# Kernel tuning notes

Hardware: AMD Instinct MI355X
Metric: run time of the kernel (lower is better)

The kernel has to match this reference:

```python
import jax, jax.numpy as jnp
import numpy as np
from jax import lax

B, C, H, W = 1, 128, 56, 56
NH, NG, KS = 4, 1, 3
CG = C // NG          # channels per group
CH = C // NH          # channels per head
NHG = NH // NG        # heads per group
SCALE = CH ** -0.5


def _norm_grid(h, w, n):
    # matches _get_normalized_grid: (y, x) order, each normalized to [-1, 1]
    y = jnp.arange(h, dtype=jnp.float32) / (h - 1.0) * 2.0 - 1.0
    x = jnp.arange(w, dtype=jnp.float32) / (w - 1.0) * 2.0 - 1.0
    g = jnp.stack(jnp.meshgrid(y, x, indexing='ij'), axis=-1)  # (h, w, 2)
    return jnp.broadcast_to(g[None], (n, h, w, 2))


def _grid_sample(img, grid):
    # F.grid_sample: bilinear, align_corners=True, zeros padding; grid is (x, y) in [-1, 1]
    n, c, hi, wi = img.shape
    gs = grid.shape[1:-1]
    gx = grid[..., 0].reshape(n, -1)
    gy = grid[..., 1].reshape(n, -1)
    fx = (gx + 1.0) * 0.5 * (wi - 1)
    fy = (gy + 1.0) * 0.5 * (hi - 1)
    x0 = jnp.floor(fx)
    y0 = jnp.floor(fy)
    wx = fx - x0
    wy = fy - y0
    x0 = x0.astype(jnp.int32)
    y0 = y0.astype(jnp.int32)
    imgf = img.reshape(n, c, hi * wi)

    def corner(xi, yi, wgt):
        valid = (xi >= 0) & (xi < wi) & (yi >= 0) & (yi < hi)
        idx = jnp.clip(yi, 0, hi - 1) * wi + jnp.clip(xi, 0, wi - 1)
        vals = jax.vmap(lambda im, ii: jnp.take(im, ii, axis=1))(imgf, idx)  # (n, c, P)
        return vals * (wgt * valid)[:, None, :]

    out = (corner(x0, y0, (1 - wx) * (1 - wy)) + corner(x0 + 1, y0, wx * (1 - wy))
           + corner(x0, y0 + 1, (1 - wx) * wy) + corner(x0 + 1, y0 + 1, wx * wy))
    return out.reshape((n, c) + gs)


def _conv1x1(t, w, b):
    return jnp.einsum('bchw,oc->bohw', t, w) + b[None, :, None, None]


def _forward(x, query, dw_w, dw_b, ln_w, ln_b, pw_w, k_w, k_b, v_w, v_b, out_w, out_b, rpe_table):
    # conv_offset: depthwise 3x3 (stride 1, pad 1) -> channel LayerNorm -> GELU -> 1x1 to 2ch (no bias)
    qg = query.reshape(B * NG, CG, H, W)
    t = lax.conv_general_dilated(qg, dw_w, (1, 1), ((1, 1), (1, 1)),
                                 dimension_numbers=('NCHW', 'OIHW', 'NCHW'),
                                 feature_group_count=CG) + dw_b[None, :, None, None]
    mu = t.mean(axis=1, keepdims=True)
    var = ((t - mu) ** 2).mean(axis=1, keepdims=True)
    t = (t - mu) / jnp.sqrt(var + 1e-5) * ln_w[None, :, None, None] + ln_b[None, :, None, None]
    t = jax.nn.gelu(t, approximate=False)
    offset = jnp.einsum('bchw,oc->bohw', t, pw_w)  # (BG, 2, Hk, Wk) in (y, x) order
    Hk, Wk = offset.shape[-2:]
    n_sample = Hk * Wk

    # tanh-scaled offsets (scale_offset_range=True, factor 0.5)
    rng = jnp.array([1.0 / (Hk - 1.0), 1.0 / (Wk - 1.0)], jnp.float32).reshape(1, 2, 1, 1)
    offset = jnp.tanh(offset) * rng * 0.5
    offset = jnp.transpose(offset, (0, 2, 3, 1))  # (BG, Hk, Wk, 2)

    ref = _norm_grid(Hk, Wk, B * NG)
    rwo = offset + ref  # no clamp in the scale_offset_range branch

    # sample K/V features at deformed locations
    xs = _grid_sample(x.reshape(B * NG, CG, H, W), rwo[..., ::-1])  # (BG, CG, Hk, Wk)
    xs = xs.reshape(B, C, 1, n_sample)

    q = query.reshape(B * NH, CH, H * W)
    k = _conv1x1(xs, k_w, k_b).reshape(B * NH, CH, n_sample)
    v = _conv1x1(xs, v_w, v_b).reshape(B * NH, CH, n_sample)

    attn = jnp.einsum('bcm,bcn->bmn', q, k) * SCALE  # (B*NH, HW, n_sample)

    # relative position bias via bilinear lookup of rpe_table at displacements
    rpe = jnp.broadcast_to(rpe_table[None], (B,) + rpe_table.shape).reshape(B * NG, NHG, 2 * H - 1, 2 * W - 1)
    qgrid = _norm_grid(H, W, B * NG)
    disp = (qgrid.reshape(B * NG, H * W, 2)[:, :, None, :]
            - rwo.reshape(B * NG, n_sample, 2)[:, None, :, :]) * 0.5  # (BG, HW, n_sample, 2)
    bias = _grid_sample(rpe, disp[..., ::-1]).reshape(B * NH, H * W, n_sample)

    attn = jax.nn.softmax(attn + bias, axis=2)
    out = jnp.einsum('bmn,bcn->bcm', attn, v).reshape(B, C, H, W)
    return _conv1x1(out, out_w, out_b)


def setup_inputs() -> dict:
    key = jax.random.key(0)
    ks = jax.random.split(key, 8)
    f = lambda k, sh, s=0.02: jax.random.normal(k, sh, jnp.float32) * s
    return {
        'x': jax.random.normal(ks[0], (B, C, H, W), jnp.float32),
        'query': jax.random.normal(ks[1], (B, C, H, W), jnp.float32),
        'dw_w': f(ks[2], (CG, 1, KS, KS)),
        'dw_b': jnp.zeros((CG,), jnp.float32),
        'ln_w': jnp.ones((CG,), jnp.float32),
        'ln_b': jnp.zeros((CG,), jnp.float32),
        'pw_w': f(ks[3], (2, CG)),
        'k_w': f(ks[4], (C, C)),
        'k_b': jnp.zeros((C,), jnp.float32),
        'v_w': f(ks[5], (C, C)),
        'v_b': jnp.zeros((C,), jnp.float32),
        'out_w': f(ks[6], (C, C)),
        'out_b': jnp.zeros((C,), jnp.float32),
        'rpe_table': f(ks[7], (NH, 2 * H - 1, 2 * W - 1), 0.01),
    }


def reference(x, query, dw_w, dw_b, ln_w, ln_b, pw_w, k_w, k_b, v_w, v_b, out_w, out_b, rpe_table):
    return _forward(x, query, dw_w, dw_b, ln_w, ln_b, pw_w, k_w, k_b, v_w, v_b, out_w, out_b, rpe_table)
```

## Files before the change

### kernel.cpp

```cpp
#include <hip/hip_runtime.h>
#include <hip/hip_bf16.h>
#include <math.h>

#define HH 56
#define WW 56
#define HW 3136
#define NHEAD 4
#define RP 111
#define TP 113
#define TPE 12769
#define SCALE 0.17677669529663687f
#define GHW 12544
#define NCHUNK 14
#define CLEN 224
#define NSTEP 7

typedef unsigned short ushortT;
typedef __attribute__((ext_vector_type(8))) short short8v;
typedef __attribute__((ext_vector_type(16))) float f32x16;

#define OFF_RWO  0u
#define OFF_AA   8192u
#define OFF_W4   12288u
#define OFF_KBF  24832u
#define OFF_VBF  225536u
#define OFF_QBF  426240u
#define OFF_ATT  626944u
#define OFF_KWT  1028352u
#define OFF_VWT  1044736u
#define OFF_OWT  1061120u
#define OFF_XT   1077504u
#define OFF_QT   1478912u
#define OFF_TP2  1880320u
#define OFF_PART 1982976u

__device__ __forceinline__ ushortT f2bf(float f) {
    unsigned u = __float_as_uint(f);
    u += 0x7fffu + ((u >> 16) & 1u);
    return (ushortT)(u >> 16);
}

__device__ __forceinline__ unsigned cvtpk(float lo, float hi) {
    unsigned r;
    asm("v_cvt_pk_bf16_f32 %0, %1, %2" : "=v"(r) : "v"(lo), "v"(hi));
    return r;
}

__global__ void prep_kernel(const float* __restrict__ a, const float* __restrict__ b,
                            const float* __restrict__ c, const float* __restrict__ rpe,
                            float* __restrict__ at, float* __restrict__ bt,
                            float* __restrict__ ct, float2* __restrict__ tp2) {
    int i = blockIdx.x * 256 + threadIdx.x;
    if (blockIdx.y < 3) {
        if (i >= 16384) return;
        const float* src = (blockIdx.y == 0) ? a : (blockIdx.y == 1) ? b : c;
        float* dst       = (blockIdx.y == 0) ? at : (blockIdx.y == 1) ? bt : ct;
        int o = i >> 7, cc = i & 127;
        dst[cc * 128 + o] = src[i];
    } else {
        if (i >= NHEAD * TPE) return;
        int hd = i / TPE, r = i % TPE;
        int py = r / TP, px = r % TP;
        float v0 = 0.f, v1 = 0.f;
        if (py >= 1 && py <= RP) {
            if (px >= 1 && px <= RP)     v0 = rpe[hd * RP * RP + (py - 1) * RP + (px - 1)];
            if (px + 1 >= 1 && px + 1 <= RP) v1 = rpe[hd * RP * RP + (py - 1) * RP + px];
        }
        tp2[i] = make_float2(v0, v1);
    }
}

__global__ __launch_bounds__(256) void tx_kernel(const float* __restrict__ x,
                                                 const float* __restrict__ query,
                                                 float* __restrict__ xT, float* __restrict__ qT,
                                                 ushortT* __restrict__ qbf) {
    const float* src = blockIdx.z ? query : x;
    float* dst       = blockIdx.z ? qT : xT;
    __shared__ float tile[32][33];
    int pt = blockIdx.x * 32;
    int ct = blockIdx.y * 32;
    int jj = threadIdx.x & 31, ii = threadIdx.x >> 5;
#pragma unroll
    for (int r = 0; r < 4; r++)
        tile[ii + r * 8][jj] = src[(ct + ii + r * 8) * HW + pt + jj];
    __syncthreads();
#pragma unroll
    for (int r = 0; r < 4; r++) {
        int p = pt + ii + r * 8, c = ct + jj;
        float val = tile[jj][ii + r * 8];
        dst[p * 128 + c] = val;
        if (blockIdx.z)
            qbf[(size_t)((c >> 5) * HW + p) * 32 + (c & 31)] = f2bf(val * SCALE);
    }
}

__device__ __forceinline__ float wave_sum(float v) {
#pragma unroll
    for (int o = 1; o < 64; o <<= 1) v += __shfl_xor(v, o);
    return v;
}

__global__ __launch_bounds__(128) void offset_kernel(
    const float* __restrict__ qT, const float* __restrict__ dww, const float* __restrict__ dwb,
    const float* __restrict__ lnw, const float* __restrict__ lnb, const float* __restrict__ pww,
    float* __restrict__ rwo, int* __restrict__ aa, float* __restrict__ w4) {
    int p = blockIdx.x;
    int c = threadIdx.x;
    int h = p / WW, w = p % WW;

    float t = dwb[c];
#pragma unroll
    for (int ky = 0; ky < 3; ky++) {
        int yy = h + ky - 1;
        if ((unsigned)yy < (unsigned)HH) {
#pragma unroll
            for (int kx = 0; kx < 3; kx++) {
                int xx = w + kx - 1;
                if ((unsigned)xx < (unsigned)WW)
                    t += qT[(yy * WW + xx) * 128 + c] * dww[c * 9 + ky * 3 + kx];
            }
        }
    }

    __shared__ float sred[4];
    int wid = c >> 6, lane0 = ((c & 63) == 0);

    float s = wave_sum(t);
    if (lane0) sred[wid] = s;
    __syncthreads();
    float mu = (sred[0] + sred[1]) * (1.f / 128.f);
    float d = t - mu;
    __syncthreads();
    s = wave_sum(d * d);
    if (lane0) sred[wid] = s;
    __syncthreads();
    float var = (sred[0] + sred[1]) * (1.f / 128.f);

    float tn = d / sqrtf(var + 1e-5f) * lnw[c] + lnb[c];
    float g = 0.5f * tn * (1.f + erff(tn * 0.70710678118654752f));

    float sy = wave_sum(g * pww[c]);
    float sx = wave_sum(g * pww[128 + c]);
    __syncthreads();
    if (lane0) { sred[wid] = sy; sred[2 + wid] = sx; }
    __syncthreads();
    if (c == 0) {
        float thy = tanhf(sred[0] + sred[1]);
        float thx = tanhf(sred[2] + sred[3]);
        rwo[p * 2]     = thy * (0.5f / 55.f) + ((float)h * (2.f / 55.f) - 1.f);
        rwo[p * 2 + 1] = thx * (0.5f / 55.f) + ((float)w * (2.f / 55.f) - 1.f);
        float ty = 55.f - (float)h - 0.25f * thy;
        float tx = 55.f - (float)w - 0.25f * thx;
        float tyf = floorf(ty), txf = floorf(tx);
        float wy = ty - tyf, wx = tx - txf;
        aa[p] = ((int)tyf) * TP + (int)txf + TP + 1;
        float4 wv;
        wv.x = (1.f - wx) * (1.f - wy);
        wv.y = wx * (1.f - wy);
        wv.z = (1.f - wx) * wy;
        wv.w = wx * wy;
        ((float4*)w4)[p] = wv;
    }
}

__global__ __launch_bounds__(128) void sample_kv_kernel(
    const float* __restrict__ xT, const float* __restrict__ rwo,
    const float* __restrict__ kwT, const float* __restrict__ vwT,
    const float* __restrict__ kb, const float* __restrict__ vb,
    ushortT* __restrict__ kbf, ushortT* __restrict__ vbf) {
    int n0 = blockIdx.x * 8;
    int tid = threadIdx.x;

    __shared__ float xs[128 * 9];
    __shared__ int   cidx[8][4];
    __shared__ float cw[8][4];
    __shared__ ushortT kst[8][128];

    if (tid < 8) {
        int n = n0 + tid;
        float gy = rwo[2 * n], gx = rwo[2 * n + 1];
        float fx = (gx + 1.f) * 27.5f;
        float fy = (gy + 1.f) * 27.5f;
        float x0f = floorf(fx), y0f = floorf(fy);
        float wx = fx - x0f, wy = fy - y0f;
        int x0 = (int)x0f, y0 = (int)y0f;
#pragma unroll
        for (int k = 0; k < 4; k++) {
            int xi = x0 + (k & 1), yi = y0 + (k >> 1);
            float wgt = ((k & 1) ? wx : 1.f - wx) * ((k >> 1) ? wy : 1.f - wy);
            bool v = (xi >= 0) && (xi < WW) && (yi >= 0) && (yi < HH);
            cidx[tid][k] = min(max(yi, 0), HH - 1) * WW + min(max(xi, 0), WW - 1);
            cw[tid][k] = v ? wgt : 0.f;
        }
    }
    __syncthreads();

#pragma unroll
    for (int j = 0; j < 8; j++) {
        float s = cw[j][0] * xT[cidx[j][0] * 128 + tid]
                + cw[j][1] * xT[cidx[j][1] * 128 + tid]
                + cw[j][2] * xT[cidx[j][2] * 128 + tid]
                + cw[j][3] * xT[cidx[j][3] * 128 + tid];
        xs[tid * 9 + j] = s;
    }
    __syncthreads();

    float ak[8], av[8];
#pragma unroll
    for (int j = 0; j < 8; j++) { ak[j] = 0.f; av[j] = 0.f; }
    for (int c = 0; c < 128; c++) {
        float wk = kwT[c * 128 + tid];
        float wv = vwT[c * 128 + tid];
#pragma unroll
        for (int j = 0; j < 8; j++) {
            float xv = xs[c * 9 + j];
            ak[j] += wk * xv;
            av[j] += wv * xv;
        }
    }
    float kbv = kb[tid], vbv = vb[tid];
    int hh = tid >> 5, ch = tid & 31;

    unsigned vp[4];
#pragma unroll
    for (int q = 0; q < 4; q++)
        vp[q] = (unsigned)f2bf(av[2 * q] + vbv) | ((unsigned)f2bf(av[2 * q + 1] + vbv) << 16);
    *(uint4*)(vbf + (size_t)(hh * 32 + ch) * HW + n0) = make_uint4(vp[0], vp[1], vp[2], vp[3]);

#pragma unroll
    for (int j = 0; j < 8; j++) kst[j][tid] = f2bf(ak[j] + kbv);
    __syncthreads();
#pragma unroll
    for (int r = 0; r < 4; r++) {
        int lin = tid + 128 * r;
        int j = lin >> 6, dd = lin & 63;
        int o = 2 * dd;
        unsigned val = *(unsigned*)&kst[j][o];
        int hd2 = o >> 5, ch2 = o & 31;
        ((unsigned*)kbf)[((size_t)(hd2 * HW + n0 + j) * 32 + ch2) >> 1] = val;
    }
}

__device__ __forceinline__ void mkw(float pa0, float pa1, float pb0, float pb1, int h,
                                    unsigned &wlo, unsigned &whi) {
    float ta0 = __shfl_xor(pa0, 32);
    float ta1 = __shfl_xor(pa1, 32);
    float tb0 = __shfl_xor(pb0, 32);
    float tb1 = __shfl_xor(pb1, 32);
    wlo = cvtpk(h ? tb0 : pa0, h ? tb1 : pa1);
    whi = cvtpk(h ? pb0 : ta0, h ? pb1 : ta1);
}

__global__ __launch_bounds__(256) void attn_kernel(
    const ushortT* __restrict__ qbf, const ushortT* __restrict__ kbf,
    const ushortT* __restrict__ vbf,
    const int* __restrict__ aa, const float4* __restrict__ w4,
    const float2* __restrict__ tp2g, float* __restrict__ part) {
    const int chunk = blockIdx.x;
    const int mtile = blockIdx.y;
    const int hd = blockIdx.z;
    const int tid = threadIdx.x;
    const int wv = tid >> 6;
    const int l = tid & 63;
    const int lm = l & 31;
    const int h = l >> 5;

    const int start = chunk * CLEN;
    const int m0w = mtile * 128 + wv * 32;
    const int mg = m0w + lm;
    const int mc = (mg < HW) ? mg : (HW - 1);

    __shared__ int aa_s[CLEN];
    __shared__ float4 w4_s[CLEN];
    __shared__ float obuf[4][32][33];

    if (tid < CLEN) { aa_s[tid] = aa[start + tid]; w4_s[tid] = ((const float4*)w4)[start + tid]; }
    __syncthreads();

    const int base_m = (mc / WW) * TP + (mc % WW);
    const float2* __restrict__ tp2 = tp2g + hd * TPE;

    const ushortT* qb = qbf + (size_t)(hd * HW + mc) * 32 + h * 8;
    short8v qf0 = *(const short8v*)(qb);
    short8v qf1 = *(const short8v*)(qb + 16);

    const ushortT* kbp = kbf + (size_t)(hd * HW + start) * 32;
    const ushortT* vbp = vbf + (size_t)(hd * 32 + lm) * HW + start;

    f32x16 accO;
#pragma unroll
    for (int i = 0; i < 16; i++) accO[i] = 0.f;
    float ssum = 0.f;

    for (int nt = 0; nt < NSTEP; ++nt) {
        const ushortT* ka = kbp + (size_t)(nt * 32 + lm) * 32 + h * 8;
        short8v kf0 = *(const short8v*)(ka);
        short8v kf1 = *(const short8v*)(ka + 16);
        f32x16 s;
#pragma unroll
        for (int i = 0; i < 16; i++) s[i] = 0.f;
        s = __builtin_amdgcn_mfma_f32_32x32x16_bf16(kf0, qf0, s, 0, 0, 0);
        s = __builtin_amdgcn_mfma_f32_32x32x16_bf16(kf1, qf1, s, 0, 0, 0);

        float p[16];
#pragma unroll
        for (int r = 0; r < 16; ++r) {
            int nl = nt * 32 + (r & 3) + 8 * (r >> 2) + 4 * h;
            int a0 = aa_s[nl] + base_m;
            float4 wvv = w4_s[nl];
            float2 t01 = tp2[a0];
            float2 t23 = tp2[a0 + TP];
            float bias = wvv.x * t01.x + wvv.y * t01.y + wvv.z * t23.x + wvv.w * t23.y;
            float pr = __expf(s[r] + bias);
            ssum += pr;
            p[r] = pr;
        }

        union { unsigned u[4]; short8v s8; } A0, A1;
        mkw(p[0], p[1], p[4], p[5], h, A0.u[0], A0.u[2]);
        mkw(p[2], p[3], p[6], p[7], h, A0.u[1], A0.u[3]);
        mkw(p[8], p[9], p[12], p[13], h, A1.u[0], A1.u[2]);
        mkw(p[10], p[11], p[14], p[15], h, A1.u[1], A1.u[3]);

        const ushortT* va = vbp + nt * 32 + h * 8;
        short8v vf0 = *(const short8v*)(va);
        short8v vf1 = *(const short8v*)(va + 16);
        accO = __builtin_amdgcn_mfma_f32_32x32x16_bf16(A0.s8, vf0, accO, 0, 0, 0);
        accO = __builtin_amdgcn_mfma_f32_32x32x16_bf16(A1.s8, vf1, accO, 0, 0, 0);
    }

    float st = ssum + __shfl_xor(ssum, 32);

#pragma unroll
    for (int r = 0; r < 16; ++r) {
        int mr = (r & 3) + 8 * (r >> 2) + 4 * h;
        obuf[wv][mr][lm] = accO[r];
    }
    __syncthreads();

    float* pbase = part + (size_t)(chunk * 33) * GHW + hd * HW;
    if (mg < HW) {
        if (h == 0) pbase[mg] = st;
        int c0 = h * 16;
#pragma unroll
        for (int k = 0; k < 4; ++k) {
            float4 o4 = *(const float4*)&obuf[wv][lm][c0 + 4 * k];
            pbase[(size_t)(1 + c0 + 4 * k + 0) * GHW + mg] = o4.x;
            pbase[(size_t)(1 + c0 + 4 * k + 1) * GHW + mg] = o4.y;
            pbase[(size_t)(1 + c0 + 4 * k + 2) * GHW + mg] = o4.z;
            pbase[(size_t)(1 + c0 + 4 * k + 3) * GHW + mg] = o4.w;
        }
    }
}

__global__ __launch_bounds__(256) void combine_kernel(const float* __restrict__ part,
                                                      float* __restrict__ att, int nchunk) {
    int g = blockIdx.x * 256 + threadIdx.x;
    int c0 = blockIdx.y * 8;
    int hd = g / HW, m = g % HW;
    const float* pb = part + g;

    float s = 0.f;
    float a[8];
#pragma unroll
    for (int cc = 0; cc < 8; cc++) a[cc] = 0.f;
    for (int k = 0; k < nchunk; k++) {
        s += pb[(size_t)(k * 33) * GHW];
#pragma unroll
        for (int cc = 0; cc < 8; cc++)
            a[cc] += pb[(size_t)(k * 33 + 1 + c0 + cc) * GHW];
    }
    float inv = 1.f / s;
#pragma unroll
    for (int cc = 0; cc < 8; cc++)
        att[(hd * 32 + c0 + cc) * HW + m] = a[cc] * inv;
}

__global__ __launch_bounds__(128) void out_conv_kernel(const float* __restrict__ att,
                                                       const float* __restrict__ owT,
                                                       const float* __restrict__ ob,
                                                       float* __restrict__ out) {
    int m0 = blockIdx.x * 8;
    int tid = threadIdx.x;
    __shared__ float at[128 * 9];
    for (int e = tid; e < 1024; e += 128) {
        int c = e >> 3, j = e & 7;
        at[c * 9 + j] = att[c * HW + m0 + j];
    }
    __syncthreads();

    float a[8];
#pragma unroll
    for (int j = 0; j < 8; j++) a[j] = 0.f;
    for (int c = 0; c < 128; c++) {
        float w = owT[c * 128 + tid];
#pragma unroll
        for (int j = 0; j < 8; j++) a[j] += w * at[c * 9 + j];
    }
    float b = ob[tid];
#pragma unroll
    for (int j = 0; j < 8; j++) out[tid * HW + m0 + j] = a[j] + b;
}

extern "C" void kernel_launch(void* const* d_in, const int* in_sizes, int n_in,
                              void* d_out, int out_size, void* d_ws, size_t ws_size,
                              hipStream_t stream) {
    const float* x     = (const float*)d_in[0];
    const float* query = (const float*)d_in[1];
    const float* dww   = (const float*)d_in[2];
    const float* dwb   = (const float*)d_in[3];
    const float* lnw   = (const float*)d_in[4];
    const float* lnb   = (const float*)d_in[5];
    const float* pww   = (const float*)d_in[6];
    const float* kw    = (const float*)d_in[7];
    const float* kb    = (const float*)d_in[8];
    const float* vw    = (const float*)d_in[9];
    const float* vb    = (const float*)d_in[10];
    const float* ow    = (const float*)d_in[11];
    const float* ob    = (const float*)d_in[12];
    const float* rpe   = (const float*)d_in[13];
    float* out = (float*)d_out;
    float* ws  = (float*)d_ws;

    prep_kernel<<<dim3(200, 4), 256, 0, stream>>>(kw, vw, ow, rpe,
                                                  ws + OFF_KWT, ws + OFF_VWT, ws + OFF_OWT,
                                                  (float2*)(ws + OFF_TP2));
    tx_kernel<<<dim3(98, 4, 2), 256, 0, stream>>>(x, query, ws + OFF_XT, ws + OFF_QT,
                                                  (ushortT*)(ws + OFF_QBF));
    offset_kernel<<<HW, 128, 0, stream>>>(ws + OFF_QT, dww, dwb, lnw, lnb, pww,
                                          ws + OFF_RWO, (int*)(ws + OFF_AA), ws + OFF_W4);
    sample_kv_kernel<<<392, 128, 0, stream>>>(ws + OFF_XT, ws + OFF_RWO,
                                              ws + OFF_KWT, ws + OFF_VWT, kb, vb,
                                              (ushortT*)(ws + OFF_KBF), (ushortT*)(ws + OFF_VBF));
    attn_kernel<<<dim3(NCHUNK, 25, NHEAD), 256, 0, stream>>>(
        (const ushortT*)(ws + OFF_QBF), (const ushortT*)(ws + OFF_KBF),
        (const ushortT*)(ws + OFF_VBF),
        (const int*)(ws + OFF_AA), (const float4*)(ws + OFF_W4),
        (const float2*)(ws + OFF_TP2), ws + OFF_PART);
    combine_kernel<<<dim3(49, 4), 256, 0, stream>>>(ws + OFF_PART, ws + OFF_ATT, NCHUNK);
    out_conv_kernel<<<392, 128, 0, stream>>>(ws + OFF_ATT, ws + OFF_OWT, ob, out);
}
```

Measured before the change: 195.5 us.

## Fuse prep kernels, stage RPE window in LDS, use exp2, merge combine with out conv

The weight/rpe prep and transpose kernels are merged into one launch, and the combine and output 1x1 conv kernels are fused so the normalized attention never goes through global memory. The attention kernel now uses 128-thread blocks of 64 queries and computes the range of RPE table rows the chunk touches. It copies that window into shared memory so bias gathers read LDS instead of global. Softmax switches to native exp2, with log2e folded into the query scale and RPE table. This cuts launches and global gathers, at the cost of more blocks and extra per-block LDS staging, and it relies on the row window fitting in the fixed 12-row buffer.

```diff
diff --git a/kernel.cpp b/kernel.cpp
--- a/kernel.cpp
+++ b/kernel.cpp
@@ -10,6 +10,8 @@
 #define TP 113
 #define TPE 12769
 #define SCALE 0.17677669529663687f
+#define LOG2E 1.44269504088896f
+#define QSC (SCALE * LOG2E)
 #define GHW 12544
 #define NCHUNK 14
 #define CLEN 224
@@ -25,7 +27,6 @@
 #define OFF_KBF  24832u
 #define OFF_VBF  225536u
 #define OFF_QBF  426240u
-#define OFF_ATT  626944u
 #define OFF_KWT  1028352u
 #define OFF_VWT  1044736u
 #define OFF_OWT  1061120u
@@ -46,51 +47,56 @@
     return r;
 }
 
-__global__ void prep_kernel(const float* __restrict__ a, const float* __restrict__ b,
-                            const float* __restrict__ c, const float* __restrict__ rpe,
-                            float* __restrict__ at, float* __restrict__ bt,
-                            float* __restrict__ ct, float2* __restrict__ tp2) {
-    int i = blockIdx.x * 256 + threadIdx.x;
-    if (blockIdx.y < 3) {
+__device__ __forceinline__ float fexp2(float x) {
+    float r;
+    asm("v_exp_f32 %0, %1" : "=v"(r) : "v"(x));
+    return r;
+}
+
+__global__ __launch_bounds__(256) void prep_all_kernel(
+    const float* __restrict__ kw, const float* __restrict__ vw, const float* __restrict__ ow,
+    const float* __restrict__ rpe, const float* __restrict__ x, const float* __restrict__ query,
+    float* __restrict__ kwT, float* __restrict__ vwT, float* __restrict__ owT,
+    float2* __restrict__ tp2, float* __restrict__ xT, float* __restrict__ qT,
+    ushortT* __restrict__ qbf) {
+    const int job = blockIdx.y;
+    __shared__ float tile[32][33];
+    if (job < 3) {
+        int i = blockIdx.x * 256 + threadIdx.x;
         if (i >= 16384) return;
-        const float* src = (blockIdx.y == 0) ? a : (blockIdx.y == 1) ? b : c;
-        float* dst       = (blockIdx.y == 0) ? at : (blockIdx.y == 1) ? bt : ct;
-        int o = i >> 7, cc = i & 127;
-        dst[cc * 128 + o] = src[i];
-    } else {
+        const float* srcw = (job == 0) ? kw : (job == 1) ? vw : ow;
+        float* dstw       = (job == 0) ? kwT : (job == 1) ? vwT : owT;
+        dstw[(i & 127) * 128 + (i >> 7)] = srcw[i];
+    } else if (job == 3) {
+        int i = blockIdx.x * 256 + threadIdx.x;
         if (i >= NHEAD * TPE) return;
         int hd = i / TPE, r = i % TPE;
         int py = r / TP, px = r % TP;
         float v0 = 0.f, v1 = 0.f;
         if (py >= 1 && py <= RP) {
-            if (px >= 1 && px <= RP)     v0 = rpe[hd * RP * RP + (py - 1) * RP + (px - 1)];
-            if (px + 1 >= 1 && px + 1 <= RP) v1 = rpe[hd * RP * RP + (py - 1) * RP + px];
+            if (px >= 1 && px <= RP) v0 = rpe[hd * RP * RP + (py - 1) * RP + (px - 1)] * LOG2E;
+            if (px <= RP - 1)        v1 = rpe[hd * RP * RP + (py - 1) * RP + px] * LOG2E;
         }
         tp2[i] = make_float2(v0, v1);
-    }
-}
-
-__global__ __launch_bounds__(256) void tx_kernel(const float* __restrict__ x,
-                                                 const float* __restrict__ query,
-                                                 float* __restrict__ xT, float* __restrict__ qT,
-                                                 ushortT* __restrict__ qbf) {
-    const float* src = blockIdx.z ? query : x;
-    float* dst       = blockIdx.z ? qT : xT;
-    __shared__ float tile[32][33];
-    int pt = blockIdx.x * 32;
-    int ct = blockIdx.y * 32;
-    int jj = threadIdx.x & 31, ii = threadIdx.x >> 5;
-#pragma unroll
-    for (int r = 0; r < 4; r++)
-        tile[ii + r * 8][jj] = src[(ct + ii + r * 8) * HW + pt + jj];
-    __syncthreads();
-#pragma unroll
-    for (int r = 0; r < 4; r++) {
-        int p = pt + ii + r * 8, c = ct + jj;
-        float val = tile[jj][ii + r * 8];
-        dst[p * 128 + c] = val;
-        if (blockIdx.z)
-            qbf[(size_t)((c >> 5) * HW + p) * 32 + (c & 31)] = f2bf(val * SCALE);
+    } else {
+        int bx = blockIdx.x;
+        if (bx >= 392) return;
+        const float* src = (job == 5) ? query : x;
+        float* dst       = (job == 5) ? qT : xT;
+        int pt = (bx % 98) * 32, ct = (bx / 98) * 32;
+        int jj = threadIdx.x & 31, ii = threadIdx.x >> 5;
+#pragma unroll
+        for (int r = 0; r < 4; r++)
+            tile[ii + r * 8][jj] = src[(ct + ii + r * 8) * HW + pt + jj];
+        __syncthreads();
+#pragma unroll
+        for (int r = 0; r < 4; r++) {
+            int p = pt + ii + r * 8, cc = ct + jj;
+            float val = tile[jj][ii + r * 8];
+            dst[p * 128 + cc] = val;
+            if (job == 5)
+                qbf[(size_t)((cc >> 5) * HW + p) * 32 + (cc & 31)] = f2bf(val * QSC);
+        }
     }
 }
 
@@ -251,7 +257,7 @@
     whi = cvtpk(h ? pb0 : ta0, h ? pb1 : ta1);
 }
 
-__global__ __launch_bounds__(256) void attn_kernel(
+__global__ __launch_bounds__(128) void attn_kernel(
     const ushortT* __restrict__ qbf, const ushortT* __restrict__ kbf,
     const ushortT* __restrict__ vbf,
     const int* __restrict__ aa, const float4* __restrict__ w4,
@@ -266,21 +272,47 @@
     const int h = l >> 5;
 
     const int start = chunk * CLEN;
-    const int m0w = mtile * 128 + wv * 32;
-    const int mg = m0w + lm;
-    const int mc = (mg < HW) ? mg : (HW - 1);
+    const int mg = mtile * 64 + wv * 32 + lm;
 
     __shared__ int aa_s[CLEN];
     __shared__ float4 w4_s[CLEN];
-    __shared__ float obuf[4][32][33];
-
-    if (tid < CLEN) { aa_s[tid] = aa[start + tid]; w4_s[tid] = ((const float4*)w4)[start + tid]; }
-    __syncthreads();
-
-    const int base_m = (mc / WW) * TP + (mc % WW);
-    const float2* __restrict__ tp2 = tp2g + hd * TPE;
-
-    const ushortT* qb = qbf + (size_t)(hd * HW + mc) * 32 + h * 8;
+    __shared__ float ubuf[12 * TP * 2];
+    __shared__ int sred[4];
+    float2* tpw = (float2*)ubuf;
+    float* obuf = ubuf;
+
+    int rmin = 1 << 20, rmax = -(1 << 20);
+    for (int i = tid; i < CLEN; i += 128) {
+        int av = aa[start + i];
+        aa_s[i] = av;
+        w4_s[i] = w4[start + i];
+        int row = (av * 37118) >> 22;
+        rmin = min(rmin, row);
+        rmax = max(rmax, row);
+    }
+#pragma unroll
+    for (int o = 1; o < 64; o <<= 1) {
+        rmin = min(rmin, __shfl_xor(rmin, o));
+        rmax = max(rmax, __shfl_xor(rmax, o));
+    }
+    if (l == 0) { sred[wv] = rmin; sred[2 + wv] = rmax; }
+    __syncthreads();
+    rmin = min(sred[0], sred[1]);
+    rmax = max(sred[2], sred[3]);
+    const int rm0 = (mtile * 64) / WW;
+    const int rm1 = (mtile * 64 + 63) / WW;
+    const int R0 = rmin + rm0;
+    const int NR = rmax + rm1 + 2 - R0;
+
+    const float2* srcw = tp2g + hd * TPE + R0 * TP;
+    for (int i = tid; i < NR * TP; i += 128) tpw[i] = srcw[i];
+    const int rbase = R0 * TP;
+    for (int i = tid; i < CLEN; i += 128) aa_s[i] -= rbase;
+    __syncthreads();
+
+    const int base_m = (mg / WW) * TP + (mg % WW);
+
+    const ushortT* qb = qbf + (size_t)(hd * HW + mg) * 32 + h * 8;
     short8v qf0 = *(const short8v*)(qb);
     short8v qf1 = *(const short8v*)(qb + 16);
 
@@ -308,10 +340,10 @@
             int nl = nt * 32 + (r & 3) + 8 * (r >> 2) + 4 * h;
             int a0 = aa_s[nl] + base_m;
             float4 wvv = w4_s[nl];
-            float2 t01 = tp2[a0];
-            float2 t23 = tp2[a0 + TP];
+            float2 t01 = tpw[a0];
+            float2 t23 = tpw[a0 + TP];
             float bias = wvv.x * t01.x + wvv.y * t01.y + wvv.z * t23.x + wvv.w * t23.y;
-            float pr = __expf(s[r] + bias);
+            float pr = fexp2(s[r] + bias);
             ssum += pr;
             p[r] = pr;
         }
@@ -331,75 +363,75 @@
 
     float st = ssum + __shfl_xor(ssum, 32);
 
+    __syncthreads();
 #pragma unroll
     for (int r = 0; r < 16; ++r) {
         int mr = (r & 3) + 8 * (r >> 2) + 4 * h;
-        obuf[wv][mr][lm] = accO[r];
+        obuf[(wv * 32 + mr) * 33 + lm] = accO[r];
     }
     __syncthreads();
 
     float* pbase = part + (size_t)(chunk * 33) * GHW + hd * HW;
-    if (mg < HW) {
-        if (h == 0) pbase[mg] = st;
-        int c0 = h * 16;
-#pragma unroll
-        for (int k = 0; k < 4; ++k) {
-            float4 o4 = *(const float4*)&obuf[wv][lm][c0 + 4 * k];
-            pbase[(size_t)(1 + c0 + 4 * k + 0) * GHW + mg] = o4.x;
-            pbase[(size_t)(1 + c0 + 4 * k + 1) * GHW + mg] = o4.y;
-            pbase[(size_t)(1 + c0 + 4 * k + 2) * GHW + mg] = o4.z;
-            pbase[(size_t)(1 + c0 + 4 * k + 3) * GHW + mg] = o4.w;
-        }
-    }
-}
-
-__global__ __launch_bounds__(256) void combine_kernel(const float* __restrict__ part,
-                                                      float* __restrict__ att, int nchunk) {
-    int g = blockIdx.x * 256 + threadIdx.x;
-    int c0 = blockIdx.y * 8;
-    int hd = g / HW, m = g % HW;
-    const float* pb = part + g;
-
-    float s = 0.f;
-    float a[8];
-#pragma unroll
-    for (int cc = 0; cc < 8; cc++) a[cc] = 0.f;
-    for (int k = 0; k < nchunk; k++) {
-        s += pb[(size_t)(k * 33) * GHW];
-#pragma unroll
-        for (int cc = 0; cc < 8; cc++)
-            a[cc] += pb[(size_t)(k * 33 + 1 + c0 + cc) * GHW];
-    }
-    float inv = 1.f / s;
-#pragma unroll
-    for (int cc = 0; cc < 8; cc++)
-        att[(hd * 32 + c0 + cc) * HW + m] = a[cc] * inv;
-}
-
-__global__ __launch_bounds__(128) void out_conv_kernel(const float* __restrict__ att,
-                                                       const float* __restrict__ owT,
-                                                       const float* __restrict__ ob,
-                                                       float* __restrict__ out) {
+    if (h == 0) pbase[mg] = st;
+    int c0 = h * 16;
+#pragma unroll
+    for (int k = 0; k < 4; ++k) {
+        float4 o4 = *(const float4*)&obuf[(wv * 32 + lm) * 33 + c0 + 4 * k];
+        pbase[(size_t)(1 + c0 + 4 * k + 0) * GHW + mg] = o4.x;
+        pbase[(size_t)(1 + c0 + 4 * k + 1) * GHW + mg] = o4.y;
+        pbase[(size_t)(1 + c0 + 4 * k + 2) * GHW + mg] = o4.z;
+        pbase[(size_t)(1 + c0 + 4 * k + 3) * GHW + mg] = o4.w;
+    }
+}
+
+__global__ __launch_bounds__(128) void combine_out_kernel(
+    const float* __restrict__ part, const float* __restrict__ owT,
+    const float* __restrict__ ob, float* __restrict__ out) {
     int m0 = blockIdx.x * 8;
     int tid = threadIdx.x;
+    int hd = tid >> 5, c = tid & 31;
+
     __shared__ float at[128 * 9];
-    for (int e = tid; e < 1024; e += 128) {
-        int c = e >> 3, j = e & 7;
-        at[c * 9 + j] = att[c * HW + m0 + j];
-    }
-    __syncthreads();
+    __shared__ float inv_s[4][8];
 
     float a[8];
 #pragma unroll
     for (int j = 0; j < 8; j++) a[j] = 0.f;
-    for (int c = 0; c < 128; c++) {
-        float w = owT[c * 128 + tid];
-#pragma unroll
-        for (int j = 0; j < 8; j++) a[j] += w * at[c * 9 + j];
+    for (int k = 0; k < NCHUNK; k++) {
+        const float* p = part + (size_t)(k * 33 + 1 + c) * GHW + hd * HW + m0;
+        float4 x0 = *(const float4*)p, x1 = *(const float4*)(p + 4);
+        a[0] += x0.x; a[1] += x0.y; a[2] += x0.z; a[3] += x0.w;
+        a[4] += x1.x; a[5] += x1.y; a[6] += x1.z; a[7] += x1.w;
+    }
+    if (c == 0) {
+        float sm[8];
+#pragma unroll
+        for (int j = 0; j < 8; j++) sm[j] = 0.f;
+        for (int k = 0; k < NCHUNK; k++) {
+            const float* p = part + (size_t)(k * 33) * GHW + hd * HW + m0;
+            float4 x0 = *(const float4*)p, x1 = *(const float4*)(p + 4);
+            sm[0] += x0.x; sm[1] += x0.y; sm[2] += x0.z; sm[3] += x0.w;
+            sm[4] += x1.x; sm[5] += x1.y; sm[6] += x1.z; sm[7] += x1.w;
+        }
+#pragma unroll
+        for (int j = 0; j < 8; j++) inv_s[hd][j] = 1.f / sm[j];
+    }
+    __syncthreads();
+#pragma unroll
+    for (int j = 0; j < 8; j++) at[tid * 9 + j] = a[j] * inv_s[hd][j];
+    __syncthreads();
+
+    float acc[8];
+#pragma unroll
+    for (int j = 0; j < 8; j++) acc[j] = 0.f;
+    for (int cc = 0; cc < 128; cc++) {
+        float w = owT[cc * 128 + tid];
+#pragma unroll
+        for (int j = 0; j < 8; j++) acc[j] += w * at[cc * 9 + j];
     }
     float b = ob[tid];
 #pragma unroll
-    for (int j = 0; j < 8; j++) out[tid * HW + m0 + j] = a[j] + b;
+    for (int j = 0; j < 8; j++) out[tid * HW + m0 + j] = acc[j] + b;
 }
 
 extern "C" void kernel_launch(void* const* d_in, const int* in_sizes, int n_in,
@@ -422,21 +454,19 @@
     float* out = (float*)d_out;
     float* ws  = (float*)d_ws;
 
-    prep_kernel<<<dim3(200, 4), 256, 0, stream>>>(kw, vw, ow, rpe,
-                                                  ws + OFF_KWT, ws + OFF_VWT, ws + OFF_OWT,
-                                                  (float2*)(ws + OFF_TP2));
-    tx_kernel<<<dim3(98, 4, 2), 256, 0, stream>>>(x, query, ws + OFF_XT, ws + OFF_QT,
-                                                  (ushortT*)(ws + OFF_QBF));
+    prep_all_kernel<<<dim3(392, 6), 256, 0, stream>>>(
+        kw, vw, ow, rpe, x, query,
+        ws + OFF_KWT, ws + OFF_VWT, ws + OFF_OWT, (float2*)(ws + OFF_TP2),
+        ws + OFF_XT, ws + OFF_QT, (ushortT*)(ws + OFF_QBF));
     offset_kernel<<<HW, 128, 0, stream>>>(ws + OFF_QT, dww, dwb, lnw, lnb, pww,
                                           ws + OFF_RWO, (int*)(ws + OFF_AA), ws + OFF_W4);
     sample_kv_kernel<<<392, 128, 0, stream>>>(ws + OFF_XT, ws + OFF_RWO,
                                               ws + OFF_KWT, ws + OFF_VWT, kb, vb,
                                               (ushortT*)(ws + OFF_KBF), (ushortT*)(ws + OFF_VBF));
-    attn_kernel<<<dim3(NCHUNK, 25, NHEAD), 256, 0, stream>>>(
+    attn_kernel<<<dim3(NCHUNK, 49, NHEAD), 128, 0, stream>>>(
         (const ushortT*)(ws + OFF_QBF), (const ushortT*)(ws + OFF_KBF),
         (const ushortT*)(ws + OFF_VBF),
         (const int*)(ws + OFF_AA), (const float4*)(ws + OFF_W4),
         (const float2*)(ws + OFF_TP2), ws + OFF_PART);
-    combine_kernel<<<dim3(49, 4), 256, 0, stream>>>(ws + OFF_PART, ws + OFF_ATT, NCHUNK);
-    out_conv_kernel<<<392, 128, 0, stream>>>(ws + OFF_ATT, ws + OFF_OWT, ob, out);
-}
+    combine_out_kernel<<<392, 128, 0, stream>>>(ws + OFF_PART, ws + OFF_OWT, ob, out);
+}
```

Result: faster. 168.6 us (-13.7%).
